# Optimization experiments

Hardware: AMD Instinct MI355X
Metric: run time of the kernel (lower is better)

## Reference

```python
import jax, jax.numpy as jnp
import numpy as np

N_SPECIES = 119
N_RADIAL = 5
N_BASIS = 7
R_MIN = 0.5
R_MAX = 6.0
UNITS = (512, 512)
EMB_NORM = 1.0 / np.sqrt(N_BASIS)
N_ATOMS = 20000
N_PAIRS = 800000
N_FEAT = 360  # gaussian moments for n_radial=5, n_contr=8

# triangular index sets for symmetric contractions
_t2i, _t2j = np.tril_indices(N_RADIAL)  # 15 unique (r,s) pairs
_t3 = np.array([(i, j, k) for i in range(N_RADIAL) for j in range(i + 1) for k in range(j + 1)])
_t3i, _t3j, _t3k = _t3[:, 0], _t3[:, 1], _t3[:, 2]  # 35 unique (r,s,t) triples


def _forward(R, Z, neighbor, offsets, embeddings, W1, b1, W2, b2, W3, b3):
    n_atoms = R.shape[0]
    idx_i, idx_j = neighbor[0], neighbor[1]
    # --- distance computation (free space, init_box == 0) ---
    dr_vec = R[idx_j] - R[idx_i] + offsets                      # (P,3)
    dr = jnp.sqrt(jnp.sum(dr_vec * dr_vec, axis=-1))            # (P,)
    dn = dr_vec / (dr + 1e-5)[:, None]                          # unit vectors
    # --- gaussian radial basis + species-pair embedding + cosine cutoff ---
    shifts = jnp.linspace(R_MIN, R_MAX, N_BASIS)
    betta = N_BASIS ** 2 / R_MAX ** 2
    rad_norm = (2.0 * betta / np.pi) ** 0.75
    basis = rad_norm * jnp.exp(-betta * (dr[:, None] - shifts) ** 2)   # (P,B)
    cutoff = 0.5 * (jnp.cos(np.pi * dr / R_MAX) + 1.0) * (dr < R_MAX)
    emb = embeddings[Z[idx_j], Z[idx_i]]                               # (P,R,B)
    radial = EMB_NORM * jnp.einsum('prb,pb->pr', emb, basis) * cutoff[:, None]  # (P,R)
    # --- geometric moments, aggregated per central atom ---
    m1 = radial[:, :, None] * dn[:, None, :]                    # (P,R,3)
    m2 = m1[..., None] * dn[:, None, None, :]                   # (P,R,3,3)
    m3 = m2[..., None] * dn[:, None, None, None, :]             # (P,R,3,3,3)
    seg = lambda x: jax.ops.segment_sum(x, idx_i, num_segments=n_atoms)
    M0, M1, M2, M3 = seg(radial), seg(m1), seg(m2), seg(m3)
    # --- invariant contractions (gaussian moments) ---
    c1 = jnp.einsum('ari,asi->ars', M1, M1)[:, _t2i, _t2j]
    c2 = jnp.einsum('arij,asij->ars', M2, M2)[:, _t2i, _t2j]
    c3 = jnp.einsum('arijk,asijk->ars', M3, M3)[:, _t2i, _t2j]
    c4 = jnp.einsum('arij,asik,atjk->arst', M2, M2, M2)[:, _t3i, _t3j, _t3k]
    c5 = jnp.einsum('ari,asj,atij->arst', M1, M1, M2)[:, _t2i, _t2j].reshape(n_atoms, -1)
    c6 = jnp.einsum('arijk,asijl,atkl->arst', M3, M3, M2)[:, _t2i, _t2j].reshape(n_atoms, -1)
    c7 = jnp.einsum('arijk,asij,atk->arst', M3, M2, M1).reshape(n_atoms, -1)
    feats = jnp.concatenate([M0, c1, c2, c3, c4, c5, c6, c7], axis=-1)  # (A,360)
    # --- vmapped per-atom NTK readout MLP (swish) ---
    h = jax.nn.swish(feats @ W1 / np.sqrt(N_FEAT) + 0.1 * b1)
    h = jax.nn.swish(h @ W2 / np.sqrt(UNITS[0]) + 0.1 * b2)
    out = h @ W3 / np.sqrt(UNITS[1]) + 0.1 * b3                 # (A,1)
    # --- mask padded atoms (Z == 0) ---
    out = out * (Z > 0)[:, None]
    return out


def setup_inputs() -> dict:
    key = jax.random.key(0)
    ks = jax.random.split(key, 8)
    R = jax.random.uniform(ks[0], (N_ATOMS, 3), jnp.float32) * 12.0  # 12 A cube
    Z = jax.random.randint(ks[1], (N_ATOMS,), 0, N_SPECIES, jnp.int32)
    neighbor = jax.random.randint(ks[2], (2, N_PAIRS), 0, N_ATOMS, jnp.int32)
    # avoid degenerate self pairs (dr == 0 would NaN the unit vector grad)
    idx_i, idx_j = neighbor[0], neighbor[1]
    idx_j = jnp.where(idx_j == idx_i, (idx_j + 1) % N_ATOMS, idx_j)
    neighbor = jnp.stack([idx_i, idx_j], axis=0)
    box = jnp.zeros((3, 3), jnp.float32)
    offsets = jnp.zeros((N_PAIRS, 3), jnp.float32)
    embeddings = jax.random.normal(ks[3], (N_SPECIES, N_SPECIES, N_RADIAL, N_BASIS), jnp.float32)
    W1 = jax.random.normal(ks[4], (N_FEAT, UNITS[0]), jnp.float32)
    b1 = jnp.zeros((UNITS[0],), jnp.float32)
    W2 = jax.random.normal(ks[5], (UNITS[0], UNITS[1]), jnp.float32)
    b2 = jnp.zeros((UNITS[1],), jnp.float32)
    W3 = jax.random.normal(ks[6], (UNITS[1], 1), jnp.float32)
    b3 = jnp.zeros((1,), jnp.float32)
    return dict(R=R, Z=Z, neighbor=neighbor, box=box, offsets=offsets,
                embeddings=embeddings, W1=W1, b1=b1, W2=W2, b2=b2, W3=W3, b3=b3)


def reference(R, Z, neighbor, box, offsets, embeddings, W1, b1, W2, b2, W3, b3):
    # box is unused: init_box == 0 selects the free-space displacement fn
    return _forward(R, Z, neighbor, offsets, embeddings, W1, b1, W2, b2, W3, b3)
```

## Files before the change

### kernel.cpp

```cpp
#include <hip/hip_runtime.h>
#include <hip/hip_bf16.h>
#include <cmath>

#define NSP 119
#define UNITS 512
#define NFEAT 360
#define KP1 384
#define CAP 128

typedef __attribute__((ext_vector_type(8))) short short8;
typedef __attribute__((ext_vector_type(4))) float floatx4;

#define AS1 __attribute__((address_space(1)))
#define AS3 __attribute__((address_space(3)))

__device__ __forceinline__ void gload_lds16(const void* g, void* l) {
    __builtin_amdgcn_global_load_lds((AS1 void*)(size_t)g, (AS3 void*)l, 16, 0, 0);
}

__device__ __host__ constexpr int s2c(int i, int j) {
    return (i > j) ? i*(i+1)/2 + j : j*(j+1)/2 + i;
}
__device__ __host__ constexpr int s3c(int x, int y, int z) {
    int A = x > y ? x : y; A = A > z ? A : z;
    int C = x < y ? x : y; C = C < z ? C : z;
    int B = x + y + z - A - C;
    return A*(A+1)*(A+2)/6 + B*(B+1)/2 + C;
}

struct BasisConsts {
    float f0k;
    float kg;
    float scale;
    float c[6];
};

__global__ __launch_bounds__(256) void pair_prep_kernel(
    const float* __restrict__ R, const int* __restrict__ Z,
    const int* __restrict__ nbr, const float* __restrict__ offsets,
    const float* __restrict__ emb, int* __restrict__ counts,
    float* __restrict__ tmpRec, int npairs, BasisConsts bc,
    const float* __restrict__ W1, const float* __restrict__ W2,
    __hip_bfloat16* __restrict__ W1t, __hip_bfloat16* __restrict__ W2t,
    float* __restrict__ outbuf, const float* __restrict__ b3,
    int pgrid, int natoms)
{
    int blk = blockIdx.x;
    if (blk >= pgrid) {
        int b = blk - pgrid;
        if (b < 448) {
            __shared__ float tile[32][33];
            const float* W; __hip_bfloat16* Wt; int K, Kp, ik, in;
            if (b < 192) { W = W1; Wt = W1t; K = NFEAT; Kp = KP1; ik = b % 12; in = b / 12; }
            else { int b2 = b - 192; W = W2; Wt = W2t; K = UNITS; Kp = UNITS; ik = b2 & 15; in = b2 >> 4; }
            int tx = threadIdx.x & 31, ty = threadIdx.x >> 5;
            int n = in * 32 + tx;
            #pragma unroll
            for (int pp = 0; pp < 4; ++pp) {
                int kk = ty + pp * 8;
                int k = ik * 32 + kk;
                tile[kk][tx] = (k < K) ? W[(size_t)k * UNITS + n] : 0.f;
            }
            __syncthreads();
            #pragma unroll
            for (int pp = 0; pp < 4; ++pp) {
                int nn = ty + pp * 8;
                Wt[(size_t)(in * 32 + nn) * Kp + ik * 32 + tx] = __float2bfloat16(tile[tx][nn]);
            }
        } else {
            int idx = (b - 448) * 256 + threadIdx.x;
            if (idx < natoms)
                outbuf[idx] = (Z[idx] > 0) ? 0.1f * b3[0] : 0.f;
        }
        return;
    }

    int p = blk * 256 + threadIdx.x;
    if (p >= npairs) return;
    int i = nbr[p];
    int j = nbr[npairs + p];
    float dx = R[3*j]   - R[3*i]   + offsets[3*p];
    float dy = R[3*j+1] - R[3*i+1] + offsets[3*p+1];
    float dz = R[3*j+2] - R[3*i+2] + offsets[3*p+2];
    float dr2 = fmaf(dz, dz, fmaf(dy, dy, dx*dx));
    if (dr2 >= 36.0f) return;
    int pos = atomicAdd(&counts[i], 1);
    if (pos >= CAP) return;

    float dr  = sqrtf(dr2);
    float inv = 1.0f / (dr + 1e-5f);
    float d0  = dr - 0.5f;
    float basis[7];
    basis[0] = exp2f(bc.f0k * d0 * d0);
    float G  = exp2f(bc.kg * dr);
    float cur = basis[0];
    #pragma unroll
    for (int b = 0; b < 6; ++b) { cur *= G * bc.c[b]; basis[b+1] = cur; }
    float cut = 0.5f * (__cosf(dr * 0.52359877559829887f) + 1.0f);
    float s = bc.scale * cut;

    const float* e = emb + ((size_t)Z[j] * NSP + Z[i]) * 35;
    float ev[35];
    __builtin_memcpy(ev, e, 35 * sizeof(float));

    float rec[8];
    #pragma unroll
    for (int r = 0; r < 5; ++r) {
        float acc = 0.f;
        #pragma unroll
        for (int b = 0; b < 7; ++b) acc += ev[r*7+b] * basis[b];
        rec[r] = s * acc;
    }
    rec[5] = dx * inv; rec[6] = dy * inv; rec[7] = dz * inv;
    float4* out = (float4*)(tmpRec + ((size_t)i * CAP + pos) * 8);
    out[0] = make_float4(rec[0], rec[1], rec[2], rec[3]);
    out[1] = make_float4(rec[4], rec[5], rec[6], rec[7]);
}

#define SREC 28
__global__ __launch_bounds__(256) void moment_kernel(
    const float* __restrict__ tmpRec, const int* __restrict__ counts,
    float* __restrict__ momG, int natoms)
{
    int wv = threadIdx.x >> 6, lane = threadIdx.x & 63;
    int a = blockIdx.x * 4 + wv;
    __shared__ float stage[4][64][SREC];

    int cnt = 0;
    if (a < natoms) cnt = min(counts[a], CAP);

    int cr0, pk0;
    if (lane < 5)       { cr0 = lane;            pk0 = 0; }
    else if (lane < 20) { int c = lane - 5;      cr0 = c / 3;  pk0 = 1 + c % 3; }
    else if (lane < 50) { int c = lane - 20;     cr0 = c / 6;  pk0 = 4 + c % 6; }
    else                { int c = lane - 50;     cr0 = c / 10; pk0 = 10 + c % 10; }
    int cr1 = 0, pk1 = 0;
    if (lane < 36) { int c = 14 + lane; cr1 = c / 10; pk1 = 10 + c % 10; }

    float acc0 = 0.f, acc1 = 0.f;
    for (int base = 0; base < cnt; base += 64) {
        int m = min(64, cnt - base);
        if (lane < m) {
            const float4* pd = (const float4*)(tmpRec + ((size_t)a * CAP + base + lane) * 8);
            float4 u = pd[0], v = pd[1];
            float x = v.y, y = v.z, z = v.w;
            float s2_0 = x*x, s2_1 = y*x, s2_2 = y*y, s2_3 = z*x, s2_4 = z*y, s2_5 = z*z;
            float* st = stage[wv][lane];
            ((float4*)st)[0] = u;
            ((float4*)st)[1] = make_float4(v.x, 1.0f, x, y);
            ((float4*)st)[2] = make_float4(z, s2_0, s2_1, s2_2);
            ((float4*)st)[3] = make_float4(s2_3, s2_4, s2_5, s2_0*x);
            ((float4*)st)[4] = make_float4(s2_0*y, s2_2*x, s2_2*y, s2_0*z);
            ((float4*)st)[5] = make_float4(s2_1*z, s2_2*z, s2_5*x, s2_5*y);
            ((float4*)st)[6] = make_float4(s2_5*z, 0.f, 0.f, 0.f);
        }
        __builtin_amdgcn_wave_barrier();
        for (int q = 0; q < m; ++q) {
            const float* s = stage[wv][q];
            acc0 += s[cr0] * s[5 + pk0];
            acc1 += s[cr1] * s[5 + pk1];
        }
        __builtin_amdgcn_wave_barrier();
    }
    size_t base = (size_t)(a >> 6) * 6400 + (size_t)(a & 63);
    momG[base + (size_t)lane * 64] = acc0;
    if (lane < 36) momG[base + (size_t)(64 + lane) * 64] = acc1;
}

#define LROW 390
__global__ __launch_bounds__(256) void feat_kernel(
    const float* __restrict__ momG, __hip_bfloat16* __restrict__ feats)
{
    constexpr int cT2I[15] = {0,1,1,2,2,2,3,3,3,3,4,4,4,4,4};
    constexpr int cT2J[15] = {0,0,1,0,1,2,0,1,2,3,0,1,2,3,4};
    constexpr int cT3A[35] = {0, 1,1,1, 2,2,2,2,2,2, 3,3,3,3,3,3,3,3,3,3, 4,4,4,4,4,4,4,4,4,4,4,4,4,4,4};
    constexpr int cT3B[35] = {0, 0,1,1, 0,1,1,2,2,2, 0,1,1,2,2,2,3,3,3,3, 0,1,1,2,2,2,3,3,3,3,4,4,4,4,4};
    constexpr int cT3C[35] = {0, 0,0,1, 0,0,1,0,1,2, 0,0,1,0,1,2,0,1,2,3, 0,0,1,0,1,2,0,1,2,3,0,1,2,3,4};
    constexpr float cW2[6]  = {1.f,2.f,1.f,2.f,2.f,1.f};
    constexpr float cW3[10] = {1.f,3.f,3.f,1.f,3.f,6.f,3.f,3.f,3.f,1.f};

    __shared__ __hip_bfloat16 ldsF[64][LROW];
    int wv = threadIdx.x >> 6, lane = threadIdx.x & 63;
    const float* mg = momG + (size_t)blockIdx.x * 6400 + lane;

    #define LDM(e) mg[(e) * 64]
    #define STF(f, v) ldsF[lane][(f)] = __float2bfloat16(v)

    if (wv == 0) {
        float m3[50], m2[30];
        #pragma unroll
        for (int e = 0; e < 50; ++e) m3[e] = LDM(50 + e);
        #pragma unroll
        for (int e = 0; e < 30; ++e) m2[e] = LDM(20 + e);
        #pragma unroll
        for (int p = 0; p < 10; ++p) {
            int r = cT2I[p], s = cT2J[p];
            float B2v[9];
            #pragma unroll
            for (int z = 0; z < 3; ++z)
                #pragma unroll
                for (int w = 0; w < 3; ++w) {
                    float acc = 0.f;
                    #pragma unroll
                    for (int x = 0; x < 3; ++x)
                        #pragma unroll
                        for (int y = 0; y < 3; ++y)
                            acc += m3[r*10 + s3c(x,y,z)] * m3[s*10 + s3c(x,y,w)];
                    B2v[z*3+w] = acc;
                }
            #pragma unroll
            for (int t = 0; t < 5; ++t) {
                float acc = 0.f;
                #pragma unroll
                for (int z = 0; z < 3; ++z)
                    #pragma unroll
                    for (int w = 0; w < 3; ++w)
                        acc += B2v[z*3+w] * m2[t*6 + s2c(z,w)];
                STF(160 + p*5 + t, acc);
            }
        }
    } else if (wv == 1) {
        float m0[5], m1[15], m2[30];
        #pragma unroll
        for (int e = 0; e < 5; ++e)  m0[e] = LDM(e);
        #pragma unroll
        for (int e = 0; e < 15; ++e) m1[e] = LDM(5 + e);
        #pragma unroll
        for (int e = 0; e < 30; ++e) m2[e] = LDM(20 + e);
        #pragma unroll
        for (int r = 0; r < 5; ++r) STF(r, m0[r]);
        #pragma unroll
        for (int p = 0; p < 15; ++p) {
            int r = cT2I[p], s = cT2J[p];
            float v1 = m1[r*3]*m1[s*3] + m1[r*3+1]*m1[s*3+1] + m1[r*3+2]*m1[s*3+2];
            STF(5 + p, v1);
            float v2 = 0.f;
            #pragma unroll
            for (int k = 0; k < 6; ++k) v2 += cW2[k] * m2[r*6+k] * m2[s*6+k];
            STF(20 + p, v2);
        }
        #pragma unroll
        for (int q = 0; q < 35; ++q) {
            int r = cT3A[q], s = cT3B[q], t = cT3C[q];
            float v = 0.f;
            #pragma unroll
            for (int x = 0; x < 3; ++x)
                #pragma unroll
                for (int y = 0; y < 3; ++y) {
                    float d = 0.f;
                    #pragma unroll
                    for (int z = 0; z < 3; ++z)
                        d += m2[s*6 + s2c(x,z)] * m2[t*6 + s2c(y,z)];
                    v += m2[r*6 + s2c(x,y)] * d;
                }
            STF(50 + q, v);
        }
        #pragma unroll
        for (int f = NFEAT; f < KP1; ++f) STF(f, 0.f);
    } else if (wv == 2) {
        float m1[15], m2[30], m3[50];
        #pragma unroll
        for (int e = 0; e < 15; ++e) m1[e] = LDM(5 + e);
        #pragma unroll
        for (int e = 0; e < 30; ++e) m2[e] = LDM(20 + e);
        #pragma unroll
        for (int e = 0; e < 50; ++e) m3[e] = LDM(50 + e);
        #pragma unroll
        for (int p = 10; p < 15; ++p) {
            int r = cT2I[p], s = cT2J[p];
            float B2v[9];
            #pragma unroll
            for (int z = 0; z < 3; ++z)
                #pragma unroll
                for (int w = 0; w < 3; ++w) {
                    float acc = 0.f;
                    #pragma unroll
                    for (int x = 0; x < 3; ++x)
                        #pragma unroll
                        for (int y = 0; y < 3; ++y)
                            acc += m3[r*10 + s3c(x,y,z)] * m3[s*10 + s3c(x,y,w)];
                    B2v[z*3+w] = acc;
                }
            #pragma unroll
            for (int t = 0; t < 5; ++t) {
                float acc = 0.f;
                #pragma unroll
                for (int z = 0; z < 3; ++z)
                    #pragma unroll
                    for (int w = 0; w < 3; ++w)
                        acc += B2v[z*3+w] * m2[t*6 + s2c(z,w)];
                STF(160 + p*5 + t, acc);
            }
        }
        #pragma unroll
        for (int p = 0; p < 15; ++p) {
            int r = cT2I[p], s = cT2J[p];
            float o[9];
            #pragma unroll
            for (int x = 0; x < 3; ++x)
                #pragma unroll
                for (int y = 0; y < 3; ++y) o[x*3+y] = m1[r*3+x] * m1[s*3+y];
            #pragma unroll
            for (int t = 0; t < 5; ++t) {
                float v = 0.f;
                #pragma unroll
                for (int x = 0; x < 3; ++x)
                    #pragma unroll
                    for (int y = 0; y < 3; ++y)
                        v += o[x*3+y] * m2[t*6 + s2c(x,y)];
                STF(85 + p*5 + t, v);
            }
        }
    } else {
        float m1[15], m2[30], m3[50];
        #pragma unroll
        for (int e = 0; e < 15; ++e) m1[e] = LDM(5 + e);
        #pragma unroll
        for (int e = 0; e < 30; ++e) m2[e] = LDM(20 + e);
        #pragma unroll
        for (int e = 0; e < 50; ++e) m3[e] = LDM(50 + e);
        #pragma unroll
        for (int p = 0; p < 15; ++p) {
            int r = cT2I[p], s = cT2J[p];
            float v = 0.f;
            #pragma unroll
            for (int k = 0; k < 10; ++k) v += cW3[k] * m3[r*10+k] * m3[s*10+k];
            STF(35 + p, v);
        }
        #pragma unroll
        for (int r = 0; r < 5; ++r)
            #pragma unroll
            for (int s = 0; s < 5; ++s) {
                float A3z[3];
                #pragma unroll
                for (int z = 0; z < 3; ++z) {
                    float v = 0.f;
                    #pragma unroll
                    for (int x = 0; x < 3; ++x)
                        #pragma unroll
                        for (int y = 0; y < 3; ++y)
                            v += m3[r*10 + s3c(x,y,z)] * m2[s*6 + s2c(x,y)];
                    A3z[z] = v;
                }
                #pragma unroll
                for (int t = 0; t < 5; ++t) {
                    float v = A3z[0]*m1[t*3] + A3z[1]*m1[t*3+1] + A3z[2]*m1[t*3+2];
                    STF(235 + r*25 + s*5 + t, v);
                }
            }
    }
    __syncthreads();

    __hip_bfloat16* dst = feats + (size_t)blockIdx.x * 64 * KP1;
    #pragma unroll
    for (int rr = 0; rr < 16; ++rr) {
        int row = wv * 16 + rr;
        #pragma unroll
        for (int it = 0; it < 3; ++it) {
            uint32_t v = *(const uint32_t*)&ldsF[row][(it*64 + lane)*2];
            *(uint32_t*)&dst[(size_t)row * KP1 + (size_t)(it*64 + lane)*2] = v;
        }
    }
    #undef LDM
    #undef STF
}

__global__ __launch_bounds__(256) void gemm_mfma_swish(
    const __hip_bfloat16* __restrict__ A, const __hip_bfloat16* __restrict__ Bt,
    const float* __restrict__ bias, __hip_bfloat16* __restrict__ C,
    const float* __restrict__ w3, float* __restrict__ outacc,
    const int* __restrict__ Zmask,
    int Kp, int M, int Mtiles, float alpha, float a3, int fuse)
{
    __shared__ float4 As[2][1024];
    __shared__ float4 Bs[2][1024];
    int tid = threadIdx.x;
    int wave = tid >> 6, lane = tid & 63;
    int quad = lane >> 4, l16 = lane & 15;
    int wm = wave >> 1, wn = wave & 1;
    int bid = blockIdx.x;
    int mt = (bid >> 5) * 8 + (bid & 7);
    int nt = (bid >> 3) & 3;
    if (mt >= Mtiles) return;
    int rowBase = mt * 128;
    int colBase = nt * 128;

    floatx4 acc[4][4] = {};

    int srow[4], schunk[4];
    #pragma unroll
    for (int p = 0; p < 4; ++p) {
        int slot = p * 256 + tid;
        int r = slot >> 3, c = slot & 7;
        srow[p] = r;
        schunk[p] = (c & 4) | ((c & 3) ^ ((r >> 1) & 3));
    }
    const char* gA[4]; const char* gB[4];
    #pragma unroll
    for (int p = 0; p < 4; ++p) {
        gA[p] = (const char*)A  + ((size_t)(rowBase + srow[p]) * Kp) * 2 + schunk[p] * 16;
        gB[p] = (const char*)Bt + ((size_t)(colBase + srow[p]) * Kp) * 2 + schunk[p] * 16;
    }
    char* lA = (char*)As;
    char* lB = (char*)Bs;
    int wvoff = wave << 10;

    int posA[4], posB[4];
    #pragma unroll
    for (int t = 0; t < 4; ++t) {
        int rr = wm * 64 + t * 16 + l16;
        posA[t] = rr * 8 + (quad ^ ((rr >> 1) & 3));
    }
    #pragma unroll
    for (int u = 0; u < 4; ++u) {
        int cc = wn * 64 + u * 16 + l16;
        posB[u] = cc * 8 + (quad ^ ((cc >> 1) & 3));
    }

    int nK = Kp >> 6;

    #pragma unroll
    for (int p = 0; p < 4; ++p) {
        int lo = (p << 12) + wvoff;
        gload_lds16(gA[p], lA + lo);
        gload_lds16(gB[p], lB + lo);
    }
    __syncthreads();

    for (int kt = 0; kt < nK; ++kt) {
        int buf = kt & 1;
        if (kt + 1 < nK) {
            int go = (kt + 1) << 7;
            int lbase = ((buf ^ 1) << 14) + wvoff;
            #pragma unroll
            for (int p = 0; p < 4; ++p) {
                int lo = lbase + (p << 12);
                gload_lds16(gA[p] + go, lA + lo);
                gload_lds16(gB[p] + go, lB + lo);
            }
        }
        #pragma unroll
        for (int s = 0; s < 2; ++s) {
            short8 af[4], bf[4];
            #pragma unroll
            for (int t = 0; t < 4; ++t) af[t] = *(const short8*)(As[buf] + posA[t] + s * 4);
            #pragma unroll
            for (int u = 0; u < 4; ++u) bf[u] = *(const short8*)(Bs[buf] + posB[u] + s * 4);
            #pragma unroll
            for (int t = 0; t < 4; ++t)
                #pragma unroll
                for (int u = 0; u < 4; ++u)
                    acc[t][u] = __builtin_amdgcn_mfma_f32_16x16x32_bf16(
                        af[t], bf[u], acc[t][u], 0, 0, 0);
        }
        __syncthreads();
    }

    if (!fuse) {
        #pragma unroll
        for (int u = 0; u < 4; ++u) {
            int col = colBase + wn * 64 + u * 16 + l16;
            float bc = 0.1f * bias[col];
            #pragma unroll
            for (int t = 0; t < 4; ++t) {
                int row0 = rowBase + wm * 64 + t * 16 + quad * 4;
                #pragma unroll
                for (int r = 0; r < 4; ++r) {
                    float x = alpha * acc[t][u][r] + bc;
                    float v = x / (1.f + expf(-x));
                    C[(size_t)(row0 + r) * UNITS + col] = __float2bfloat16(v);
                }
            }
        }
    } else {
        float rowsum[4][4] = {};
        #pragma unroll
        for (int u = 0; u < 4; ++u) {
            int col = colBase + wn * 64 + u * 16 + l16;
            float bc = 0.1f * bias[col];
            float w3c = w3[col] * a3;
            #pragma unroll
            for (int t = 0; t < 4; ++t)
                #pragma unroll
                for (int r = 0; r < 4; ++r) {
                    float x = alpha * acc[t][u][r] + bc;
                    float v = x / (1.f + expf(-x));
                    rowsum[t][r] += v * w3c;
                }
        }
        #pragma unroll
        for (int t = 0; t < 4; ++t)
            #pragma unroll
            for (int r = 0; r < 4; ++r) {
                float s = rowsum[t][r];
                s += __shfl_xor(s, 1, 64);
                s += __shfl_xor(s, 2, 64);
                s += __shfl_xor(s, 4, 64);
                s += __shfl_xor(s, 8, 64);
                rowsum[t][r] = s;
            }
        if (l16 == 0) {
            #pragma unroll
            for (int t = 0; t < 4; ++t) {
                int row0 = rowBase + wm * 64 + t * 16 + quad * 4;
                #pragma unroll
                for (int r = 0; r < 4; ++r) {
                    int row = row0 + r;
                    if (row < M && Zmask[row] > 0)
                        atomicAdd(&outacc[row], rowsum[t][r]);
                }
            }
        }
    }
}

static inline size_t align_up(size_t x, size_t a) { return (x + a - 1) & ~(a - 1); }

extern "C" void kernel_launch(void* const* d_in, const int* in_sizes, int n_in,
                              void* d_out, int out_size, void* d_ws, size_t ws_size,
                              hipStream_t stream)
{
    const float* R       = (const float*)d_in[0];
    const int*   Z       = (const int*)  d_in[1];
    const int*   nbr     = (const int*)  d_in[2];
    const float* offsets = (const float*)d_in[4];
    const float* emb     = (const float*)d_in[5];
    const float* W1      = (const float*)d_in[6];
    const float* b1      = (const float*)d_in[7];
    const float* W2      = (const float*)d_in[8];
    const float* b2      = (const float*)d_in[9];
    const float* W3      = (const float*)d_in[10];
    const float* b3      = (const float*)d_in[11];

    int natoms = in_sizes[0] / 3;
    int npairs = in_sizes[2] / 2;
    int Mpad = ((natoms + 127) / 128) * 128;
    int Mtiles = Mpad / 128;

    char* ws = (char*)d_ws;
    size_t off = 0;
    int* counts = (int*)(ws + off); off = align_up(off + natoms*4, 256);
    float* tmpRec = (float*)(ws + off); off = align_up(off + (size_t)natoms*CAP*8*4, 256);
    float* momG = (float*)(ws + off); off = align_up(off + (size_t)Mpad*100*4, 256);
    __hip_bfloat16* W1t   = (__hip_bfloat16*)(ws + off); off = align_up(off + (size_t)UNITS*KP1*2, 256);
    __hip_bfloat16* W2t   = (__hip_bfloat16*)(ws + off); off = align_up(off + (size_t)UNITS*UNITS*2, 256);
    __hip_bfloat16* feats = (__hip_bfloat16*)(ws + off); off = align_up(off + (size_t)Mpad*KP1*2, 256);
    __hip_bfloat16* h1    = (__hip_bfloat16*)(ws + off); off = align_up(off + (size_t)Mpad*UNITS*2, 256);

    BasisConsts bc;
    {
        const double betta = 49.0 / 36.0;
        const double delta = 5.5 / 6.0;
        const double log2e = 1.4426950408889634073599246810;
        bc.f0k = (float)(-betta * log2e);
        bc.kg  = (float)(2.0 * betta * delta * log2e);
        for (int b = 0; b < 6; ++b)
            bc.c[b] = (float)exp(-betta * delta * (1.0 + delta * (2*b + 1)));
        bc.scale = (float)(pow(2.0 * betta / M_PI, 0.75) / sqrt(7.0));
    }

    hipMemsetAsync(counts, 0, (size_t)natoms * sizeof(int), stream);

    int pgrid = (npairs + 255) / 256;
    int totalBlocks = pgrid + 448 + (natoms + 255) / 256;
    pair_prep_kernel<<<dim3(totalBlocks), 256, 0, stream>>>(
        R, Z, nbr, offsets, emb, counts, tmpRec, npairs, bc,
        W1, W2, W1t, W2t, (float*)d_out, b3, pgrid, natoms);

    moment_kernel<<<dim3(Mpad / 4), 256, 0, stream>>>(
        tmpRec, counts, momG, natoms);
    feat_kernel<<<dim3(Mpad / 64), 256, 0, stream>>>(momG, feats);

    float a1 = 1.0f / sqrtf((float)NFEAT);
    float a2 = 1.0f / sqrtf((float)UNITS);
    int gemmGrid = ((Mtiles + 7) / 8) * 8 * 4;
    gemm_mfma_swish<<<dim3(gemmGrid), 256, 0, stream>>>(
        feats, W1t, b1, h1, nullptr, nullptr, nullptr, KP1, natoms, Mtiles, a1, 0.f, 0);
    gemm_mfma_swish<<<dim3(gemmGrid), 256, 0, stream>>>(
        h1, W2t, b2, nullptr, W3, (float*)d_out, Z, UNITS, natoms, Mtiles, a2, a2, 1);
}
```

Before: 195.6 us.

## Fuse both MLP GEMMs into one kernel keeping hidden activations in LDS

Replaces the two tiled GEMM launches with one kernel per 64-row block. Layer-1 swish outputs go into a swizzled LDS buffer and feed layer 2 directly, so the h1 global round-trip and one launch disappear. The final reduction writes the output directly instead of using atomics. In exchange, A and B operands are now read straight from global memory into registers with no LDS staging, so weight tiles are re-read by every block. The 64KB LDS footprint also limits occupancy.

```diff
diff --git a/kernel.cpp b/kernel.cpp
--- a/kernel.cpp
+++ b/kernel.cpp
@@ -10,13 +10,6 @@
 
 typedef __attribute__((ext_vector_type(8))) short short8;
 typedef __attribute__((ext_vector_type(4))) float floatx4;
-
-#define AS1 __attribute__((address_space(1)))
-#define AS3 __attribute__((address_space(3)))
-
-__device__ __forceinline__ void gload_lds16(const void* g, void* l) {
-    __builtin_amdgcn_global_load_lds((AS1 void*)(size_t)g, (AS3 void*)l, 16, 0, 0);
-}
 
 __device__ __host__ constexpr int s2c(int i, int j) {
     return (i > j) ? i*(i+1)/2 + j : j*(j+1)/2 + i;
@@ -365,151 +358,157 @@
     #undef STF
 }
 
-__global__ __launch_bounds__(256) void gemm_mfma_swish(
-    const __hip_bfloat16* __restrict__ A, const __hip_bfloat16* __restrict__ Bt,
-    const float* __restrict__ bias, __hip_bfloat16* __restrict__ C,
-    const float* __restrict__ w3, float* __restrict__ outacc,
-    const int* __restrict__ Zmask,
-    int Kp, int M, int Mtiles, float alpha, float a3, int fuse)
+__global__ __launch_bounds__(256) void fused_mlp_kernel(
+    const __hip_bfloat16* __restrict__ A,
+    const __hip_bfloat16* __restrict__ W1t,
+    const __hip_bfloat16* __restrict__ W2t,
+    const float* __restrict__ b1, const float* __restrict__ b2,
+    const float* __restrict__ w3, const float* __restrict__ b3,
+    const int* __restrict__ Z, float* __restrict__ out,
+    float alpha1, float alpha2, int natoms)
 {
-    __shared__ float4 As[2][1024];
-    __shared__ float4 Bs[2][1024];
+    __shared__ __align__(16) __hip_bfloat16 h1[64 * 512];
+    __shared__ float scr[128];
     int tid = threadIdx.x;
     int wave = tid >> 6, lane = tid & 63;
     int quad = lane >> 4, l16 = lane & 15;
     int wm = wave >> 1, wn = wave & 1;
-    int bid = blockIdx.x;
-    int mt = (bid >> 5) * 8 + (bid & 7);
-    int nt = (bid >> 3) & 3;
-    if (mt >= Mtiles) return;
-    int rowBase = mt * 128;
-    int colBase = nt * 128;
-
-    floatx4 acc[4][4] = {};
-
-    int srow[4], schunk[4];
-    #pragma unroll
-    for (int p = 0; p < 4; ++p) {
-        int slot = p * 256 + tid;
-        int r = slot >> 3, c = slot & 7;
-        srow[p] = r;
-        schunk[p] = (c & 4) | ((c & 3) ^ ((r >> 1) & 3));
-    }
-    const char* gA[4]; const char* gB[4];
-    #pragma unroll
-    for (int p = 0; p < 4; ++p) {
-        gA[p] = (const char*)A  + ((size_t)(rowBase + srow[p]) * Kp) * 2 + schunk[p] * 16;
-        gB[p] = (const char*)Bt + ((size_t)(colBase + srow[p]) * Kp) * 2 + schunk[p] * 16;
-    }
-    char* lA = (char*)As;
-    char* lB = (char*)Bs;
-    int wvoff = wave << 10;
-
-    int posA[4], posB[4];
-    #pragma unroll
-    for (int t = 0; t < 4; ++t) {
-        int rr = wm * 64 + t * 16 + l16;
-        posA[t] = rr * 8 + (quad ^ ((rr >> 1) & 3));
-    }
-    #pragma unroll
-    for (int u = 0; u < 4; ++u) {
-        int cc = wn * 64 + u * 16 + l16;
-        posB[u] = cc * 8 + (quad ^ ((cc >> 1) & 3));
-    }
-
-    int nK = Kp >> 6;
-
-    #pragma unroll
-    for (int p = 0; p < 4; ++p) {
-        int lo = (p << 12) + wvoff;
-        gload_lds16(gA[p], lA + lo);
-        gload_lds16(gB[p], lB + lo);
+    int rowBase = blockIdx.x * 64;
+
+    const __hip_bfloat16* pA0 = A + (size_t)(rowBase + wm*32 + l16) * KP1 + quad*8;
+    const __hip_bfloat16* pA1 = pA0 + (size_t)16 * KP1;
+    for (int nt = 0; nt < 4; ++nt) {
+        floatx4 acc[2][4] = {};
+        const __hip_bfloat16* pB[4];
+        #pragma unroll
+        for (int u = 0; u < 4; ++u)
+            pB[u] = W1t + (size_t)(nt*128 + wn*64 + u*16 + l16) * KP1 + quad*8;
+
+        short8 ca0 = *(const short8*)pA0;
+        short8 ca1 = *(const short8*)pA1;
+        short8 cb[4];
+        #pragma unroll
+        for (int u = 0; u < 4; ++u) cb[u] = *(const short8*)pB[u];
+
+        for (int kt = 0; kt < KP1/32; ++kt) {
+            short8 na0, na1, nb[4];
+            bool more = (kt + 1 < KP1/32);
+            if (more) {
+                na0 = *(const short8*)(pA0 + (kt+1)*32);
+                na1 = *(const short8*)(pA1 + (kt+1)*32);
+                #pragma unroll
+                for (int u = 0; u < 4; ++u) nb[u] = *(const short8*)(pB[u] + (kt+1)*32);
+            }
+            #pragma unroll
+            for (int u = 0; u < 4; ++u) {
+                acc[0][u] = __builtin_amdgcn_mfma_f32_16x16x32_bf16(ca0, cb[u], acc[0][u], 0, 0, 0);
+                acc[1][u] = __builtin_amdgcn_mfma_f32_16x16x32_bf16(ca1, cb[u], acc[1][u], 0, 0, 0);
+            }
+            if (more) {
+                ca0 = na0; ca1 = na1;
+                #pragma unroll
+                for (int u = 0; u < 4; ++u) cb[u] = nb[u];
+            }
+        }
+        #pragma unroll
+        for (int u = 0; u < 4; ++u) {
+            int col = nt*128 + wn*64 + u*16 + l16;
+            float bc = 0.1f * b1[col];
+            int chunk = col >> 3, e = col & 7;
+            #pragma unroll
+            for (int t = 0; t < 2; ++t) {
+                int row0 = wm*32 + t*16 + quad*4;
+                #pragma unroll
+                for (int r = 0; r < 4; ++r) {
+                    float x = alpha1 * acc[t][u][r] + bc;
+                    float v = x / (1.f + expf(-x));
+                    int row = row0 + r;
+                    int slot = row*64 + (chunk ^ (row & 7));
+                    h1[slot*8 + e] = __float2bfloat16(v);
+                }
+            }
+        }
     }
     __syncthreads();
 
-    for (int kt = 0; kt < nK; ++kt) {
-        int buf = kt & 1;
-        if (kt + 1 < nK) {
-            int go = (kt + 1) << 7;
-            int lbase = ((buf ^ 1) << 14) + wvoff;
-            #pragma unroll
-            for (int p = 0; p < 4; ++p) {
-                int lo = lbase + (p << 12);
-                gload_lds16(gA[p] + go, lA + lo);
-                gload_lds16(gB[p] + go, lB + lo);
-            }
-        }
-        #pragma unroll
-        for (int s = 0; s < 2; ++s) {
-            short8 af[4], bf[4];
-            #pragma unroll
-            for (int t = 0; t < 4; ++t) af[t] = *(const short8*)(As[buf] + posA[t] + s * 4);
-            #pragma unroll
-            for (int u = 0; u < 4; ++u) bf[u] = *(const short8*)(Bs[buf] + posB[u] + s * 4);
-            #pragma unroll
-            for (int t = 0; t < 4; ++t)
-                #pragma unroll
-                for (int u = 0; u < 4; ++u)
-                    acc[t][u] = __builtin_amdgcn_mfma_f32_16x16x32_bf16(
-                        af[t], bf[u], acc[t][u], 0, 0, 0);
-        }
-        __syncthreads();
-    }
-
-    if (!fuse) {
+    float rowsum[2][4] = {};
+    for (int nt = 0; nt < 4; ++nt) {
+        floatx4 acc[2][4] = {};
+        const __hip_bfloat16* pB[4];
+        #pragma unroll
+        for (int u = 0; u < 4; ++u)
+            pB[u] = W2t + (size_t)(nt*128 + wn*64 + u*16 + l16) * UNITS + quad*8;
+
+        short8 cb[4];
+        #pragma unroll
+        for (int u = 0; u < 4; ++u) cb[u] = *(const short8*)pB[u];
+
+        for (int kt = 0; kt < UNITS/32; ++kt) {
+            short8 nb[4];
+            bool more = (kt + 1 < UNITS/32);
+            if (more) {
+                #pragma unroll
+                for (int u = 0; u < 4; ++u) nb[u] = *(const short8*)(pB[u] + (kt+1)*32);
+            }
+            short8 af[2];
+            #pragma unroll
+            for (int t = 0; t < 2; ++t) {
+                int row = wm*32 + t*16 + l16;
+                int slot = row*64 + ((kt*4 + quad) ^ (row & 7));
+                af[t] = *(const short8*)&h1[slot*8];
+            }
+            #pragma unroll
+            for (int u = 0; u < 4; ++u) {
+                acc[0][u] = __builtin_amdgcn_mfma_f32_16x16x32_bf16(af[0], cb[u], acc[0][u], 0, 0, 0);
+                acc[1][u] = __builtin_amdgcn_mfma_f32_16x16x32_bf16(af[1], cb[u], acc[1][u], 0, 0, 0);
+            }
+            if (more) {
+                #pragma unroll
+                for (int u = 0; u < 4; ++u) cb[u] = nb[u];
+            }
+        }
         #pragma unroll
         for (int u = 0; u < 4; ++u) {
-            int col = colBase + wn * 64 + u * 16 + l16;
-            float bc = 0.1f * bias[col];
-            #pragma unroll
-            for (int t = 0; t < 4; ++t) {
-                int row0 = rowBase + wm * 64 + t * 16 + quad * 4;
+            int col = nt*128 + wn*64 + u*16 + l16;
+            float bc = 0.1f * b2[col];
+            float w3c = w3[col] * alpha2;
+            #pragma unroll
+            for (int t = 0; t < 2; ++t)
                 #pragma unroll
                 for (int r = 0; r < 4; ++r) {
-                    float x = alpha * acc[t][u][r] + bc;
-                    float v = x / (1.f + expf(-x));
-                    C[(size_t)(row0 + r) * UNITS + col] = __float2bfloat16(v);
-                }
-            }
-        }
-    } else {
-        float rowsum[4][4] = {};
-        #pragma unroll
-        for (int u = 0; u < 4; ++u) {
-            int col = colBase + wn * 64 + u * 16 + l16;
-            float bc = 0.1f * bias[col];
-            float w3c = w3[col] * a3;
-            #pragma unroll
-            for (int t = 0; t < 4; ++t)
-                #pragma unroll
-                for (int r = 0; r < 4; ++r) {
-                    float x = alpha * acc[t][u][r] + bc;
+                    float x = alpha2 * acc[t][u][r] + bc;
                     float v = x / (1.f + expf(-x));
                     rowsum[t][r] += v * w3c;
                 }
         }
-        #pragma unroll
-        for (int t = 0; t < 4; ++t)
+    }
+
+    #pragma unroll
+    for (int t = 0; t < 2; ++t)
+        #pragma unroll
+        for (int r = 0; r < 4; ++r) {
+            float s = rowsum[t][r];
+            s += __shfl_xor(s, 1, 64);
+            s += __shfl_xor(s, 2, 64);
+            s += __shfl_xor(s, 4, 64);
+            s += __shfl_xor(s, 8, 64);
+            rowsum[t][r] = s;
+        }
+    if (l16 == 0) {
+        #pragma unroll
+        for (int t = 0; t < 2; ++t)
             #pragma unroll
             for (int r = 0; r < 4; ++r) {
-                float s = rowsum[t][r];
-                s += __shfl_xor(s, 1, 64);
-                s += __shfl_xor(s, 2, 64);
-                s += __shfl_xor(s, 4, 64);
-                s += __shfl_xor(s, 8, 64);
-                rowsum[t][r] = s;
-            }
-        if (l16 == 0) {
-            #pragma unroll
-            for (int t = 0; t < 4; ++t) {
-                int row0 = rowBase + wm * 64 + t * 16 + quad * 4;
-                #pragma unroll
-                for (int r = 0; r < 4; ++r) {
-                    int row = row0 + r;
-                    if (row < M && Zmask[row] > 0)
-                        atomicAdd(&outacc[row], rowsum[t][r]);
-                }
-            }
+                int rowLocal = wm*32 + t*16 + quad*4 + r;
+                scr[rowLocal*2 + wn] = rowsum[t][r];
+            }
+    }
+    __syncthreads();
+    if (tid < 64) {
+        int g = rowBase + tid;
+        if (g < natoms) {
+            float val = scr[tid*2] + scr[tid*2 + 1];
+            out[g] = (Z[g] > 0) ? (val + 0.1f * b3[0]) : 0.f;
         }
     }
 }
@@ -535,7 +534,6 @@
     int natoms = in_sizes[0] / 3;
     int npairs = in_sizes[2] / 2;
     int Mpad = ((natoms + 127) / 128) * 128;
-    int Mtiles = Mpad / 128;
 
     char* ws = (char*)d_ws;
     size_t off = 0;
@@ -545,7 +543,6 @@
     __hip_bfloat16* W1t   = (__hip_bfloat16*)(ws + off); off = align_up(off + (size_t)UNITS*KP1*2, 256);
     __hip_bfloat16* W2t   = (__hip_bfloat16*)(ws + off); off = align_up(off + (size_t)UNITS*UNITS*2, 256);
     __hip_bfloat16* feats = (__hip_bfloat16*)(ws + off); off = align_up(off + (size_t)Mpad*KP1*2, 256);
-    __hip_bfloat16* h1    = (__hip_bfloat16*)(ws + off); off = align_up(off + (size_t)Mpad*UNITS*2, 256);
 
     BasisConsts bc;
     {
@@ -573,9 +570,6 @@
 
     float a1 = 1.0f / sqrtf((float)NFEAT);
     float a2 = 1.0f / sqrtf((float)UNITS);
-    int gemmGrid = ((Mtiles + 7) / 8) * 8 * 4;
-    gemm_mfma_swish<<<dim3(gemmGrid), 256, 0, stream>>>(
-        feats, W1t, b1, h1, nullptr, nullptr, nullptr, KP1, natoms, Mtiles, a1, 0.f, 0);
-    gemm_mfma_swish<<<dim3(gemmGrid), 256, 0, stream>>>(
-        h1, W2t, b2, nullptr, W3, (float*)d_out, Z, UNITS, natoms, Mtiles, a2, a2, 1);
-}
+    fused_mlp_kernel<<<dim3(Mpad / 64), 256, 0, stream>>>(
+        feats, W1t, W2t, b1, b2, W3, b3, Z, (float*)d_out, a1, a2, natoms);
+}
```

New measurement: 251.2 us. +28.4%, slower.
